# Kernel optimization log

Measured on AMD Instinct MI355X. Metric: run time of the kernel, lower is better.

Reference implementation:

```python
import jax, jax.numpy as jnp
import numpy as np

NUM_EXPERTS = 8
TOP_K = 2


def setup_inputs() -> dict:
    key = jax.random.key(0)
    k1, k2 = jax.random.split(key)
    x = jax.random.normal(k1, (4, 4096, 2048), dtype=jnp.float32)
    gate_w = jax.random.normal(k2, (NUM_EXPERTS, 2048), dtype=jnp.float32) * (1.0 / np.sqrt(2048.0))
    return {"x": x, "gate_w": gate_w}


def reference(x, gate_w):
    B, T, C = x.shape
    x_flat = x.reshape(-1, C)                       # [N, C], N = B*T
    logits = jnp.einsum('nc,ec->ne', x_flat, gate_w)  # [N, E]
    probs = jax.nn.softmax(logits, axis=-1)
    weights, indices = jax.lax.top_k(probs, TOP_K)   # [N, K]
    weights = weights / jnp.sum(weights, axis=-1, keepdims=True)
    # one_hot(indices, E).sum(1): per-token multi-hot expert selection mask
    mask = jax.nn.one_hot(indices, NUM_EXPERTS, dtype=jnp.float32).sum(axis=1)  # [N, E]
    f = mask.mean(axis=0)                            # fraction of tokens per expert
    P = probs.mean(axis=0)                           # mean router prob per expert
    aux_loss = NUM_EXPERTS * jnp.sum(f * P)
    return weights, indices, aux_loss
```

## Files before the change

### kernel.cpp

```cpp
#include <hip/hip_runtime.h>

#define NTOK 16384
#define NC 2048
#define C4 512
#define NE 8
#define TPB 256
#define TOKW 2
#define TOK_PER_BLOCK 8
#define NBLK (NTOK / TOK_PER_BLOCK)
#define NBANK 64

__global__ void zero_ws_kernel(float* ws) {
    const int tid = threadIdx.x;
    #pragma unroll
    for (int i = 0; i < 4; ++i) ws[tid + i * 256] = 0.0f;
}

__global__ __launch_bounds__(TPB, 2) void router_kernel(
    const float* __restrict__ x, const float* __restrict__ gw,
    float* __restrict__ out, float* __restrict__ ws) {
    __shared__ float s_psum[NE];
    __shared__ float s_cnt[NE];

    const int tid = threadIdx.x;
    if (tid < NE) { s_psum[tid] = 0.0f; s_cnt[tid] = 0.0f; }
    __syncthreads();

    const int wave = tid >> 6;
    const int lane = tid & 63;
    const float4* x4 = (const float4*)x;
    const float4* gw4 = (const float4*)gw;
    const int t0 = blockIdx.x * TOK_PER_BLOCK + wave * TOKW;

    float* out_w = out;
    float* out_i = out + 2 * NTOK;

    float acc0[NE], acc1[NE];
    #pragma unroll
    for (int e = 0; e < NE; ++e) { acc0[e] = 0.0f; acc1[e] = 0.0f; }

    #pragma unroll 2
    for (int k = 0; k < 8; ++k) {
        const int idx = lane + k * 64;
        const float4 xv0 = x4[(size_t)t0 * C4 + idx];
        const float4 xv1 = x4[(size_t)(t0 + 1) * C4 + idx];
        #pragma unroll
        for (int e = 0; e < NE; ++e) {
            const float4 wv = gw4[e * C4 + idx];
            acc0[e] += xv0.x * wv.x + xv0.y * wv.y + xv0.z * wv.z + xv0.w * wv.w;
            acc1[e] += xv1.x * wv.x + xv1.y * wv.y + xv1.z * wv.z + xv1.w * wv.w;
        }
    }

    #pragma unroll
    for (int off = 32; off >= 1; off >>= 1) {
        #pragma unroll
        for (int e = 0; e < NE; ++e) {
            acc0[e] += __shfl_xor(acc0[e], off, 64);
            acc1[e] += __shfl_xor(acc1[e], off, 64);
        }
    }

    const int sel = lane & 1;
    float l[NE];
    #pragma unroll
    for (int e = 0; e < NE; ++e) l[e] = sel ? acc1[e] : acc0[e];

    float m = l[0];
    #pragma unroll
    for (int e = 1; e < NE; ++e) m = fmaxf(m, l[e]);
    float p[NE];
    float s = 0.0f;
    #pragma unroll
    for (int e = 0; e < NE; ++e) { p[e] = expf(l[e] - m); s += p[e]; }
    const float inv = 1.0f / s;
    #pragma unroll
    for (int e = 0; e < NE; ++e) p[e] *= inv;

    int i0 = 0; float p0 = p[0];
    #pragma unroll
    for (int e = 1; e < NE; ++e) if (p[e] > p0) { p0 = p[e]; i0 = e; }
    int i1 = (i0 == 0) ? 1 : 0; float p1 = p[i1];
    #pragma unroll
    for (int e = 0; e < NE; ++e)
        if (e != i0 && p[e] > p1) { p1 = p[e]; i1 = e; }

    if (lane < TOKW) {
        const int token = t0 + lane;
        const float wsum = p0 + p1;
        out_w[2 * token]     = p0 / wsum;
        out_w[2 * token + 1] = p1 / wsum;
        out_i[2 * token]     = (float)i0;
        out_i[2 * token + 1] = (float)i1;

        #pragma unroll
        for (int e = 0; e < NE; ++e) atomicAdd(&s_psum[e], p[e]);
        atomicAdd(&s_cnt[i0], 1.0f);
        atomicAdd(&s_cnt[i1], 1.0f);
    }

    __syncthreads();
    if (tid < NE) {
        const int bank = blockIdx.x & (NBANK - 1);
        atomicAdd(&ws[bank * 16 + tid], s_psum[tid]);
        atomicAdd(&ws[bank * 16 + NE + tid], s_cnt[tid]);
    }
}

__global__ void finalize_kernel(const float* __restrict__ ws,
                                float* __restrict__ out) {
    __shared__ float red[16];
    const int tid = threadIdx.x;
    if (tid < 16) red[tid] = 0.0f;
    __syncthreads();
    atomicAdd(&red[tid & 15], ws[tid]);
    __syncthreads();
    if (tid == 0) {
        float aux = 0.0f;
        #pragma unroll
        for (int e = 0; e < NE; ++e)
            aux += (red[NE + e] * (1.0f / NTOK)) * (red[e] * (1.0f / NTOK));
        out[4 * NTOK] = (float)NE * aux;
    }
}

extern "C" void kernel_launch(void* const* d_in, const int* in_sizes, int n_in,
                              void* d_out, int out_size, void* d_ws, size_t ws_size,
                              hipStream_t stream) {
    const float* x  = (const float*)d_in[0];
    const float* gw = (const float*)d_in[1];
    float* out = (float*)d_out;
    float* ws  = (float*)d_ws;

    zero_ws_kernel<<<1, 256, 0, stream>>>(ws);
    router_kernel<<<NBLK, TPB, 0, stream>>>(x, gw, out, ws);
    finalize_kernel<<<1, 1024, 0, stream>>>(ws, out);
}
```

Before: 43.29 us.

## Assign eight tokens per wave with 8-lane groups per token

Restructures the router dot-product so each wave processes 8 tokens, with 8 lanes per token striding over the channel dimension, instead of 2 tokens spread across all 64 lanes. This shortens the cross-lane butterfly reduction from 6 to 3 shuffle stages over fewer accumulators and cuts the block count by 4x. The per-token softmax, top-k and shared-memory atomics are spread across lanes. Each lane's x loads now stride across the row (8 consecutive float4 per token group), which may reduce coalescing per instruction, and gate weights are re-read per token group.

New measurement: 60.53 us. 39.8% more time.

```diff
diff --git a/kernel.cpp b/kernel.cpp
--- a/kernel.cpp
+++ b/kernel.cpp
@@ -5,8 +5,8 @@
 #define C4 512
 #define NE 8
 #define TPB 256
-#define TOKW 2
-#define TOK_PER_BLOCK 8
+#define TOK_PER_WAVE 8
+#define TOK_PER_BLOCK 32
 #define NBLK (NTOK / TOK_PER_BLOCK)
 #define NBANK 64
 
@@ -28,51 +28,44 @@
 
     const int wave = tid >> 6;
     const int lane = tid & 63;
-    const float4* x4 = (const float4*)x;
-    const float4* gw4 = (const float4*)gw;
-    const int t0 = blockIdx.x * TOK_PER_BLOCK + wave * TOKW;
+    const int t    = lane >> 3;
+    const int phi  = lane & 7;
+    const int token = blockIdx.x * TOK_PER_BLOCK + wave * TOK_PER_WAVE + t;
+
+    const float4* xrow = (const float4*)x + (size_t)token * C4;
+    const float4* gw4  = (const float4*)gw;
 
     float* out_w = out;
     float* out_i = out + 2 * NTOK;
 
-    float acc0[NE], acc1[NE];
+    float acc[NE];
     #pragma unroll
-    for (int e = 0; e < NE; ++e) { acc0[e] = 0.0f; acc1[e] = 0.0f; }
+    for (int e = 0; e < NE; ++e) acc[e] = 0.0f;
 
     #pragma unroll 2
-    for (int k = 0; k < 8; ++k) {
-        const int idx = lane + k * 64;
-        const float4 xv0 = x4[(size_t)t0 * C4 + idx];
-        const float4 xv1 = x4[(size_t)(t0 + 1) * C4 + idx];
+    for (int step = 0; step < C4 / 8; ++step) {
+        const int c4 = step * 8 + phi;
+        const float4 xv = xrow[c4];
         #pragma unroll
         for (int e = 0; e < NE; ++e) {
-            const float4 wv = gw4[e * C4 + idx];
-            acc0[e] += xv0.x * wv.x + xv0.y * wv.y + xv0.z * wv.z + xv0.w * wv.w;
-            acc1[e] += xv1.x * wv.x + xv1.y * wv.y + xv1.z * wv.z + xv1.w * wv.w;
+            const float4 wv = gw4[e * C4 + c4];
+            acc[e] += xv.x * wv.x + xv.y * wv.y + xv.z * wv.z + xv.w * wv.w;
         }
     }
 
     #pragma unroll
-    for (int off = 32; off >= 1; off >>= 1) {
+    for (int m = 1; m < 8; m <<= 1)
         #pragma unroll
-        for (int e = 0; e < NE; ++e) {
-            acc0[e] += __shfl_xor(acc0[e], off, 64);
-            acc1[e] += __shfl_xor(acc1[e], off, 64);
-        }
-    }
+        for (int e = 0; e < NE; ++e)
+            acc[e] += __shfl_xor(acc[e], m, 64);
 
-    const int sel = lane & 1;
-    float l[NE];
+    float mx = acc[0];
     #pragma unroll
-    for (int e = 0; e < NE; ++e) l[e] = sel ? acc1[e] : acc0[e];
-
-    float m = l[0];
-    #pragma unroll
-    for (int e = 1; e < NE; ++e) m = fmaxf(m, l[e]);
+    for (int e = 1; e < NE; ++e) mx = fmaxf(mx, acc[e]);
     float p[NE];
     float s = 0.0f;
     #pragma unroll
-    for (int e = 0; e < NE; ++e) { p[e] = expf(l[e] - m); s += p[e]; }
+    for (int e = 0; e < NE; ++e) { p[e] = expf(acc[e] - mx); s += p[e]; }
     const float inv = 1.0f / s;
     #pragma unroll
     for (int e = 0; e < NE; ++e) p[e] *= inv;
@@ -85,19 +78,25 @@
     for (int e = 0; e < NE; ++e)
         if (e != i0 && p[e] > p1) { p1 = p[e]; i1 = e; }
 
-    if (lane < TOKW) {
-        const int token = t0 + lane;
+    if (phi == 0) {
         const float wsum = p0 + p1;
         out_w[2 * token]     = p0 / wsum;
         out_w[2 * token + 1] = p1 / wsum;
         out_i[2 * token]     = (float)i0;
         out_i[2 * token + 1] = (float)i1;
+        atomicAdd(&s_cnt[i0], 1.0f);
+    }
+    if (phi == 1) atomicAdd(&s_cnt[i1], 1.0f);
 
-        #pragma unroll
-        for (int e = 0; e < NE; ++e) atomicAdd(&s_psum[e], p[e]);
-        atomicAdd(&s_cnt[i0], 1.0f);
-        atomicAdd(&s_cnt[i1], 1.0f);
-    }
+    float pphi = p[0];
+    pphi = (phi == 1) ? p[1] : pphi;
+    pphi = (phi == 2) ? p[2] : pphi;
+    pphi = (phi == 3) ? p[3] : pphi;
+    pphi = (phi == 4) ? p[4] : pphi;
+    pphi = (phi == 5) ? p[5] : pphi;
+    pphi = (phi == 6) ? p[6] : pphi;
+    pphi = (phi == 7) ? p[7] : pphi;
+    atomicAdd(&s_psum[phi], pphi);
 
     __syncthreads();
     if (tid < NE) {
```

## Process four tokens per wave and replace atomic banks with per-block partials

Applied to the files above, without the earlier changes.

Each wave now computes four tokens instead of two, so every gate-weight load is reused across more tokens and the grid is halved. The global atomic accumulation into banked workspace is replaced by plain per-block stores of the partial sums, which the finalize kernel reduces with a strided loop. This lets the zero-init kernel launch be dropped. The cost is more accumulator registers per thread, which may limit occupancy, and a larger serial reduction in the finalize kernel.

After: 43.98 us. About the same (+1.6%).

```diff
diff --git a/kernel.cpp b/kernel.cpp
--- a/kernel.cpp
+++ b/kernel.cpp
@@ -5,16 +5,9 @@
 #define C4 512
 #define NE 8
 #define TPB 256
-#define TOKW 2
-#define TOK_PER_BLOCK 8
+#define TOKW 4
+#define TOK_PER_BLOCK 16
 #define NBLK (NTOK / TOK_PER_BLOCK)
-#define NBANK 64
-
-__global__ void zero_ws_kernel(float* ws) {
-    const int tid = threadIdx.x;
-    #pragma unroll
-    for (int i = 0; i < 4; ++i) ws[tid + i * 256] = 0.0f;
-}
 
 __global__ __launch_bounds__(TPB, 2) void router_kernel(
     const float* __restrict__ x, const float* __restrict__ gw,
@@ -35,20 +28,24 @@
     float* out_w = out;
     float* out_i = out + 2 * NTOK;
 
-    float acc0[NE], acc1[NE];
+    float acc0[NE], acc1[NE], acc2[NE], acc3[NE];
     #pragma unroll
-    for (int e = 0; e < NE; ++e) { acc0[e] = 0.0f; acc1[e] = 0.0f; }
+    for (int e = 0; e < NE; ++e) { acc0[e] = 0.0f; acc1[e] = 0.0f; acc2[e] = 0.0f; acc3[e] = 0.0f; }
 
     #pragma unroll 2
     for (int k = 0; k < 8; ++k) {
         const int idx = lane + k * 64;
-        const float4 xv0 = x4[(size_t)t0 * C4 + idx];
+        const float4 xv0 = x4[(size_t)(t0 + 0) * C4 + idx];
         const float4 xv1 = x4[(size_t)(t0 + 1) * C4 + idx];
+        const float4 xv2 = x4[(size_t)(t0 + 2) * C4 + idx];
+        const float4 xv3 = x4[(size_t)(t0 + 3) * C4 + idx];
         #pragma unroll
         for (int e = 0; e < NE; ++e) {
             const float4 wv = gw4[e * C4 + idx];
             acc0[e] += xv0.x * wv.x + xv0.y * wv.y + xv0.z * wv.z + xv0.w * wv.w;
             acc1[e] += xv1.x * wv.x + xv1.y * wv.y + xv1.z * wv.z + xv1.w * wv.w;
+            acc2[e] += xv2.x * wv.x + xv2.y * wv.y + xv2.z * wv.z + xv2.w * wv.w;
+            acc3[e] += xv3.x * wv.x + xv3.y * wv.y + xv3.z * wv.z + xv3.w * wv.w;
         }
     }
 
@@ -58,21 +55,29 @@
         for (int e = 0; e < NE; ++e) {
             acc0[e] += __shfl_xor(acc0[e], off, 64);
             acc1[e] += __shfl_xor(acc1[e], off, 64);
+            acc2[e] += __shfl_xor(acc2[e], off, 64);
+            acc3[e] += __shfl_xor(acc3[e], off, 64);
         }
     }
 
-    const int sel = lane & 1;
+    const int t = lane & 3;
     float l[NE];
     #pragma unroll
-    for (int e = 0; e < NE; ++e) l[e] = sel ? acc1[e] : acc0[e];
+    for (int e = 0; e < NE; ++e) {
+        float v = acc0[e];
+        v = (t == 1) ? acc1[e] : v;
+        v = (t == 2) ? acc2[e] : v;
+        v = (t == 3) ? acc3[e] : v;
+        l[e] = v;
+    }
 
-    float m = l[0];
+    float mx = l[0];
     #pragma unroll
-    for (int e = 1; e < NE; ++e) m = fmaxf(m, l[e]);
+    for (int e = 1; e < NE; ++e) mx = fmaxf(mx, l[e]);
     float p[NE];
     float s = 0.0f;
     #pragma unroll
-    for (int e = 0; e < NE; ++e) { p[e] = expf(l[e] - m); s += p[e]; }
+    for (int e = 0; e < NE; ++e) { p[e] = expf(l[e] - mx); s += p[e]; }
     const float inv = 1.0f / s;
     #pragma unroll
     for (int e = 0; e < NE; ++e) p[e] *= inv;
@@ -100,11 +105,8 @@
     }
 
     __syncthreads();
-    if (tid < NE) {
-        const int bank = blockIdx.x & (NBANK - 1);
-        atomicAdd(&ws[bank * 16 + tid], s_psum[tid]);
-        atomicAdd(&ws[bank * 16 + NE + tid], s_cnt[tid]);
-    }
+    if (tid < NE)          ws[blockIdx.x * 16 + tid] = s_psum[tid];
+    else if (tid < 2 * NE) ws[blockIdx.x * 16 + tid] = s_cnt[tid - NE];
 }
 
 __global__ void finalize_kernel(const float* __restrict__ ws,
@@ -113,7 +115,11 @@
     const int tid = threadIdx.x;
     if (tid < 16) red[tid] = 0.0f;
     __syncthreads();
-    atomicAdd(&red[tid & 15], ws[tid]);
+    const int i = tid & 15;
+    float sum = 0.0f;
+    for (int b = (tid >> 4); b < NBLK; b += 64)
+        sum += ws[b * 16 + i];
+    atomicAdd(&red[i], sum);
     __syncthreads();
     if (tid == 0) {
         float aux = 0.0f;
@@ -132,7 +138,6 @@
     float* out = (float*)d_out;
     float* ws  = (float*)d_ws;
 
-    zero_ws_kernel<<<1, 256, 0, stream>>>(ws);
     router_kernel<<<NBLK, TPB, 0, stream>>>(x, gw, out, ws);
     finalize_kernel<<<1, 1024, 0, stream>>>(ws, out);
 }
```
